# Performance work log

Measured on AMD Instinct MI355X. Metric: run time of the kernel, lower is better.

Reference implementation:

```python
import jax, jax.numpy as jnp
import numpy as np

B, T, D = 32, 1024, 1024
N, L = 256, 768
H = 16
TE = 2048


def layernorm(x, g, b, eps=1e-5):
    m = jnp.mean(x, axis=-1, keepdims=True)
    v = jnp.var(x, axis=-1, keepdims=True)
    return (x - m) * jax.lax.rsqrt(v + eps) * g + b


def setup_inputs() -> dict:
    key = jax.random.key(0)
    ks = jax.random.split(key, 16)
    s = 0.02
    return {
        "x": jax.random.normal(ks[0], (B, T, D), jnp.float32),
        "xf": jax.random.normal(ks[1], (B, N, L), jnp.float32),
        "emb": jax.random.normal(ks[2], (B, TE), jnp.float32),
        "src_mask": jnp.ones((B, T, 1), jnp.float32),
        "cond_type": jax.random.randint(ks[3], (B, 1, 1), 0, 100),
        # LayerNorm params
        "ln_x_g": jnp.ones((D,), jnp.float32), "ln_x_b": jnp.zeros((D,), jnp.float32),
        "ln_t_g": jnp.ones((L,), jnp.float32), "ln_t_b": jnp.zeros((L,), jnp.float32),
        # Q/K/V projections
        "Wq": jax.random.normal(ks[4], (D, D), jnp.float32) * s, "bq": jnp.zeros((D,), jnp.float32),
        "Wk": jax.random.normal(ks[5], (L, D), jnp.float32) * s, "bk": jnp.zeros((D,), jnp.float32),
        "Wv": jax.random.normal(ks[6], (L, D), jnp.float32) * s, "bv": jnp.zeros((D,), jnp.float32),
        # StylizationBlock: SiLU -> Linear(TE, 2D); LayerNorm(D); SiLU -> Linear(D, D)
        "We": jax.random.normal(ks[7], (TE, 2 * D), jnp.float32) * s, "be": jnp.zeros((2 * D,), jnp.float32),
        "ln_y_g": jnp.ones((D,), jnp.float32), "ln_y_b": jnp.zeros((D,), jnp.float32),
        "Wo": jax.random.normal(ks[8], (D, D), jnp.float32) * s, "bo": jnp.zeros((D,), jnp.float32),
    }


def reference(x, xf, emb, src_mask, cond_type,
              ln_x_g, ln_x_b, ln_t_g, ln_t_b,
              Wq, bq, Wk, bk, Wv, bv,
              We, be, ln_y_g, ln_y_b, Wo, bo):
    Bh, Th, Dh = x.shape
    Nn = xf.shape[1]
    head = Dh // H

    # text condition gate: (B,1,1), constant per batch element
    tcond = (cond_type % 10 > 0).astype(x.dtype).reshape(Bh, 1, 1)

    q = (layernorm(x, ln_x_g, ln_x_b) @ Wq + bq).reshape(Bh, Th, H, head)
    xf_n = layernorm(xf, ln_t_g, ln_t_b)
    k = (xf_n @ Wk + bk).reshape(Bh, Nn, H, head)

    # B,T,N,H scores (note: no 1/sqrt(d) scaling, as in the original)
    att = jnp.einsum('bthd,bnhd->btnh', q, k)
    att = att + (1.0 - tcond.reshape(Bh, 1, 1, 1)) * -1000000.0
    att = jax.nn.softmax(att, axis=2)

    v = ((xf_n @ Wv + bv) * tcond).reshape(Bh, Nn, H, head)
    y = jnp.einsum('btnh,bnhd->bthd', att, v).reshape(Bh, Th, Dh)

    # StylizationBlock (dropout inactive in eval)
    emb_out = jax.nn.silu(emb) @ We + be            # B, 2D
    scale, shift = jnp.split(emb_out, 2, axis=-1)   # B, D each
    h = layernorm(y, ln_y_g, ln_y_b) * (1.0 + scale[:, None, :]) + shift[:, None, :]
    h = jax.nn.silu(h) @ Wo + bo
    return x + h
```

## Files before the change

### kernel.cpp

```cpp
#include <hip/hip_runtime.h>
#include <hip/hip_bf16.h>

#define DEV __device__ __forceinline__

typedef __attribute__((ext_vector_type(8))) short bf16x8;
typedef __attribute__((ext_vector_type(4))) float f32x4;
typedef __attribute__((ext_vector_type(8))) unsigned short u16x8;

DEV unsigned short f2bf(float f){
  unsigned int b = __float_as_uint(f);
  return (unsigned short)((b + 0x7fffu + ((b >> 16) & 1u)) >> 16);
}
DEV float bf2f(unsigned short u){ return __uint_as_float(((unsigned int)u)<<16); }

DEV float silu_f(float v){ return v / (1.f + __expf(-v)); }

DEV void gl_lds16(const void* g, void* l){
  __builtin_amdgcn_global_load_lds((const __attribute__((address_space(1))) void*)g,
                                   (__attribute__((address_space(3))) void*)l, 16, 0, 0);
}

__global__ __launch_bounds__(256) void ln_rows(const float* __restrict__ x,
    const float* __restrict__ g, const float* __restrict__ bt,
    unsigned short* __restrict__ out, int D, int nvec)
{
  int row = blockIdx.x, t = threadIdx.x;
  const float4* xr = (const float4*)(x + (size_t)row * D);
  float4 v = make_float4(0.f,0.f,0.f,0.f);
  if (t < nvec) v = xr[t];
  float s  = v.x+v.y+v.z+v.w;
  float s2 = v.x*v.x+v.y*v.y+v.z*v.z+v.w*v.w;
  #pragma unroll
  for (int o=32;o;o>>=1){ s += __shfl_down(s,o,64); s2 += __shfl_down(s2,o,64); }
  __shared__ float red[8];
  if ((t&63)==0){ red[t>>6]=s; red[4+(t>>6)]=s2; }
  __syncthreads();
  float fs  = red[0]+red[1]+red[2]+red[3];
  float fs2 = red[4]+red[5]+red[6]+red[7];
  float mean = fs / (float)D;
  float var  = fmaxf(fs2/(float)D - mean*mean, 0.f);
  float rstd = rsqrtf(var + 1e-5f);
  if (t < nvec){
    float4 gv = ((const float4*)g)[t];
    float4 bv = ((const float4*)bt)[t];
    ushort4 o4;
    o4.x = f2bf((v.x-mean)*rstd*gv.x + bv.x);
    o4.y = f2bf((v.y-mean)*rstd*gv.y + bv.y);
    o4.z = f2bf((v.z-mean)*rstd*gv.z + bv.z);
    o4.w = f2bf((v.w-mean)*rstd*gv.w + bv.w);
    *(ushort4*)(out + (size_t)row*D + t*4) = o4;
  }
}

__global__ __launch_bounds__(256) void wconv(const float* __restrict__ W,
    unsigned short* __restrict__ Wt, int K, int N)
{
  __shared__ float tile[32][33];
  int n0 = blockIdx.x<<5, k0 = blockIdx.y<<5;
  int tx = threadIdx.x & 31, ty = threadIdx.x >> 5;
  #pragma unroll
  for (int i=0;i<4;i++)
    tile[ty + i*8][tx] = W[(size_t)(k0 + ty + i*8)*N + n0 + tx];
  __syncthreads();
  #pragma unroll
  for (int i=0;i<4;i++)
    Wt[(size_t)(n0 + ty + i*8)*K + k0 + tx] = f2bf(tile[tx][ty + i*8]);
}

__global__ __launch_bounds__(256) void bcat(const float* __restrict__ a,
    const float* __restrict__ b, float* __restrict__ o)
{
  int i = blockIdx.x*256 + threadIdx.x;
  o[i] = (i < 1024) ? a[i] : b[i-1024];
}

template<int MH, int KS>
DEV void phase_mfma(f32x4 (&acc)[8][4], const bf16x8 (&aF)[4], const bf16x8 (&bB)[2][4]){
  __builtin_amdgcn_s_barrier();
  __builtin_amdgcn_s_setprio(1);
  #pragma unroll
  for (int i=0;i<4;i++)
    #pragma unroll
    for (int j=0;j<4;j++)
      acc[MH*4+i][j] = __builtin_amdgcn_mfma_f32_16x16x32_bf16(aF[i], bB[KS][j], acc[MH*4+i][j], 0,0,0);
  __builtin_amdgcn_s_setprio(0);
  __builtin_amdgcn_s_barrier();
}

template<int EPI>
__global__ __launch_bounds__(512,2) void gemm256(
  const unsigned char* __restrict__ A, const unsigned char* __restrict__ Wt,
  const float* __restrict__ bias, void* __restrict__ Cout,
  const float* __restrict__ Xadd, int M, int N, int K, int gxshift)
{
  __shared__ __align__(16) unsigned char lds[131072];
  const int nwg = gridDim.x;
  const int chunk = nwg >> 3;
  const int wg = blockIdx.x;
  const int lg = (wg & 7) * chunk + (wg >> 3);
  const int bx = lg & ((1<<gxshift)-1);
  const int by = lg >> gxshift;
  const int tid = threadIdx.x, w = tid>>6, lane = tid&63;
  const int l15 = lane&15, lq = lane>>4;
  const int wr = w>>2, wc = w&3;
  const int m0 = by<<8, n0 = bx<<8;
  const size_t K2 = (size_t)K<<1;
  const int NT = K>>6;

  const int srow = w*8 + (lane>>3);
  const int scs  = (((lane&7) ^ (lane>>3))<<4);

  f32x4 acc[8][4];
  f32x4 zero = {0.f,0.f,0.f,0.f};
  #pragma unroll
  for (int i=0;i<8;i++)
    #pragma unroll
    for (int j=0;j<4;j++) acc[i][j] = zero;

  auto stg = [&](int bf, int mat, int c, int t){
    const unsigned char* src = mat ? Wt : A;
    int prow = mat ? n0 : m0;
    gl_lds16(src + (size_t)(prow + c*64 + srow)*K2 + ((size_t)t<<7) + scs,
             lds + bf*65536 + mat*32768 + c*8192 + w*1024);
  };
  auto ldA = [&](int mh, int i, int ks, int bf)->bf16x8 {
    int r = wr*128 + mh*64 + i*16 + l15;
    return *(const bf16x8*)(lds + bf*65536 + r*128 + ((ks*64 + lq*16) ^ ((r&7)<<4)));
  };
  auto ldB = [&](int j, int ks, int bf)->bf16x8 {
    int r = wc*64 + j*16 + l15;
    return *(const bf16x8*)(lds + bf*65536 + 32768 + r*128 + ((ks*64 + lq*16) ^ ((r&7)<<4)));
  };

  stg(0,0,0,0); stg(0,0,2,0);
  stg(0,1,0,0); stg(0,1,1,0);
  stg(0,1,2,0); stg(0,1,3,0);
  stg(0,0,1,0); stg(0,0,3,0);
  stg(1,0,0,1); stg(1,0,2,1);
  stg(1,1,0,1); stg(1,1,1,1);

  for (int u=0; u<NT; ++u){
    const int buf = u&1, nb = buf^1;
    if (u+1 < NT) { asm volatile("s_waitcnt vmcnt(4)" ::: "memory"); }
    else          { asm volatile("s_waitcnt vmcnt(0)" ::: "memory"); }
    __builtin_amdgcn_sched_barrier(0);
    __builtin_amdgcn_s_barrier();

    bf16x8 bB[2][4];
    bf16x8 aF[4];
    #pragma unroll
    for (int j=0;j<4;j++) bB[0][j] = ldB(j,0,buf);
    #pragma unroll
    for (int i=0;i<4;i++) aF[i] = ldA(0,i,0,buf);
    if (u+1 < NT){ stg(nb,1,2,u+1); stg(nb,1,3,u+1); }
    phase_mfma<0,0>(acc, aF, bB);
    #pragma unroll
    for (int j=0;j<4;j++) bB[1][j] = ldB(j,1,buf);
    #pragma unroll
    for (int i=0;i<4;i++) aF[i] = ldA(0,i,1,buf);
    if (u+1 < NT){ stg(nb,0,1,u+1); stg(nb,0,3,u+1); }
    phase_mfma<0,1>(acc, aF, bB);
    #pragma unroll
    for (int i=0;i<4;i++) aF[i] = ldA(1,i,0,buf);
    if (u+2 < NT){ stg(buf,0,0,u+2); stg(buf,0,2,u+2); }
    phase_mfma<1,0>(acc, aF, bB);
    #pragma unroll
    for (int i=0;i<4;i++) aF[i] = ldA(1,i,1,buf);
    if (u+2 < NT){ stg(buf,1,0,u+2); stg(buf,1,1,u+2); }
    phase_mfma<1,1>(acc, aF, bB);
  }

  #pragma unroll
  for (int j=0;j<4;j++){
    int n = n0 + wc*64 + j*16 + l15;
    float bv = bias[n];
    #pragma unroll
    for (int mf=0;mf<8;mf++){
      int mb = m0 + wr*128 + mf*16 + lq*4;
      #pragma unroll
      for (int r=0;r<4;r++){
        size_t idx = (size_t)(mb+r)*N + n;
        float val = acc[mf][j][r] + bv;
        if (EPI==0) ((unsigned short*)Cout)[idx] = f2bf(val);
        else        ((float*)Cout)[idx] = Xadd[idx] + val;
      }
    }
  }
}

__global__ __launch_bounds__(256) void vtransp(const unsigned short* __restrict__ v,
                                               int vstride, unsigned char* __restrict__ vt)
{
  __shared__ __align__(16) unsigned short tile[16384];
  int h = blockIdx.x, b = blockIdx.y, tid = threadIdx.x;
  const unsigned short* src = v + (size_t)b*256*vstride + h*64;
  #pragma unroll
  for (int it=0; it<8; ++it){
    int idx = it*256 + tid;
    int n = idx>>3, dc = idx&7;
    *(f32x4*)&tile[n*64 + dc*8] = *(const f32x4*)(src + (size_t)n*vstride + dc*8);
  }
  __syncthreads();
  unsigned char* dst = vt + (size_t)(b*16+h)*32768;
  #pragma unroll
  for (int it=0; it<8; ++it){
    int idx = it*256 + tid;
    int d = idx>>5, nc = idx&31;
    u16x8 o;
    #pragma unroll
    for (int j=0;j<8;j++) o[j] = tile[(nc*8+j)*64 + d];
    *(u16x8*)(dst + d*512 + ((nc*16) ^ ((d&7)<<4))) = o;
  }
}

__global__ __launch_bounds__(256,2) void attn64(
  const unsigned char* __restrict__ qg, const unsigned char* __restrict__ kg,
  int kstride, const unsigned char* __restrict__ vtg, const int* __restrict__ cond,
  unsigned short* __restrict__ yout)
{
  __shared__ __align__(16) unsigned char lds[73728];
  const int wg = blockIdx.x;
  const int lg = (wg & 7) * 1024 + (wg >> 3);
  const int t0 = (lg & 15) * 64;
  const int h  = (lg >> 4) & 15;
  const int b  = lg >> 8;
  const int tid = threadIdx.x, w = tid>>6, lane = tid&63;
  const int l15 = lane&15, lq = lane>>4;

  const unsigned char* kbase = kg + (size_t)b*256*kstride + (size_t)h*128;
  const unsigned char* vtb   = vtg + (size_t)(b*16+h)*32768;
  #pragma unroll
  for (int i=0;i<8;i++){
    int base = (w*8+i)*1024;
    int n  = (base>>7) + (lane>>3);
    int cb = (lane&7)<<4;
    gl_lds16(kbase + (size_t)n*kstride + (cb ^ ((n&7)<<4)), lds + base);
    gl_lds16(vtb + base + lane*16, lds + 32768 + base);
  }
  const unsigned char* qbase = qg + (size_t)(b*1024 + t0)*2048 + h*128;
  #pragma unroll
  for (int i=0;i<2;i++){
    int row = i*32 + (tid>>3);
    int cs  = ((tid&7)<<4) ^ ((row&7)<<4);
    gl_lds16(qbase + (size_t)row*2048 + cs, lds + 65536 + i*4096 + w*1024);
  }
  __syncthreads();

  const int qr = w*16 + l15;
  const int qsw = (qr&7)<<4;
  bf16x8 aq0 = *(const bf16x8*)(lds + 65536 + qr*128 + ((lq*16) ^ qsw));
  bf16x8 aq1 = *(const bf16x8*)(lds + 65536 + qr*128 + ((64 + lq*16) ^ qsw));

  f32x4 zero = {0.f,0.f,0.f,0.f};
  f32x4 s[16];
  #pragma unroll
  for (int nt=0;nt<16;nt++) s[nt] = zero;
  #pragma unroll
  for (int nt=0;nt<16;nt++){
    int n = nt*16 + l15;
    int rb = n<<7, sw = (n&7)<<4;
    bf16x8 kb0 = *(const bf16x8*)(lds + rb + ((lq*16) ^ sw));
    bf16x8 kb1 = *(const bf16x8*)(lds + rb + ((64 + lq*16) ^ sw));
    s[nt] = __builtin_amdgcn_mfma_f32_16x16x32_bf16(aq0, kb0, s[nt], 0,0,0);
    s[nt] = __builtin_amdgcn_mfma_f32_16x16x32_bf16(aq1, kb1, s[nt], 0,0,0);
  }
  #pragma unroll
  for (int r=0;r<4;r++){
    float m = s[0][r];
    #pragma unroll
    for (int nt=1;nt<16;nt++) m = fmaxf(m, s[nt][r]);
    m = fmaxf(m, __shfl_xor(m,1,64));
    m = fmaxf(m, __shfl_xor(m,2,64));
    m = fmaxf(m, __shfl_xor(m,4,64));
    m = fmaxf(m, __shfl_xor(m,8,64));
    float sum = 0.f;
    #pragma unroll
    for (int nt=0;nt<16;nt++){ float p = __expf(s[nt][r]-m); s[nt][r]=p; sum+=p; }
    sum += __shfl_xor(sum,1,64);
    sum += __shfl_xor(sum,2,64);
    sum += __shfl_xor(sum,4,64);
    sum += __shfl_xor(sum,8,64);
    float inv = 1.f/sum;
    #pragma unroll
    for (int nt=0;nt<16;nt++) s[nt][r] *= inv;
  }
  __syncthreads();
  #pragma unroll
  for (int nt=0;nt<16;nt++){
    int n = nt*16 + l15;
    int nb = (n>>3)<<4, nr = (n&7)<<1;
    #pragma unroll
    for (int r=0;r<4;r++){
      int tl = w*16 + lq*4 + r;
      *(unsigned short*)(lds + tl*512 + ((nb ^ ((tl&7)<<4)) | nr)) = f2bf(s[nt][r]);
    }
  }
  __syncthreads();
  f32x4 yv[4];
  #pragma unroll
  for (int dt=0;dt<4;dt++) yv[dt] = zero;
  const int tl = w*16 + l15;
  const int swp = (tl&7)<<4;
  #pragma unroll
  for (int kc=0;kc<8;kc++){
    bf16x8 pa = *(const bf16x8*)(lds + tl*512 + ((kc*64 + lq*16) ^ swp));
    #pragma unroll
    for (int dt=0;dt<4;dt++){
      int d = dt*16 + l15;
      bf16x8 vbv = *(const bf16x8*)(lds + 32768 + d*512 + ((kc*64 + lq*16) ^ ((d&7)<<4)));
      yv[dt] = __builtin_amdgcn_mfma_f32_16x16x32_bf16(pa, vbv, yv[dt], 0,0,0);
    }
  }
  float tc = (cond[b] % 10 > 0) ? 1.f : 0.f;
  #pragma unroll
  for (int dt=0;dt<4;dt++){
    #pragma unroll
    for (int r=0;r<4;r++){
      int tt = t0 + w*16 + lq*4 + r;
      yout[(size_t)(b*1024 + tt)*1024 + h*64 + dt*16 + l15] = f2bf(yv[dt][r]*tc);
    }
  }
}

__global__ __launch_bounds__(256) void embgemm(const float* __restrict__ emb,
    const float* __restrict__ We, float* __restrict__ epart)
{
  __shared__ float a[32][128];
  int cb = blockIdx.x, ks = blockIdx.y, tid = threadIdx.x;
  int k0 = ks<<7;
  #pragma unroll
  for (int it=0; it<4; ++it){
    int fi = it*256 + tid;
    int r = fi>>5, c4 = (fi&31)<<2;
    float4 vv = *(const float4*)(emb + (size_t)r*2048 + k0 + c4);
    vv.x = silu_f(vv.x); vv.y = silu_f(vv.y); vv.z = silu_f(vv.z); vv.w = silu_f(vv.w);
    *(float4*)&a[r][c4] = vv;
  }
  __syncthreads();
  int c0 = (cb<<8) + tid;
  float acc[32];
  #pragma unroll
  for (int r=0;r<32;r++) acc[r]=0.f;
  for (int kk=0;kk<128;kk++){
    float wv = We[(size_t)(k0+kk)*2048 + c0];
    #pragma unroll
    for (int r=0;r<32;r++) acc[r] += a[r][kk]*wv;
  }
  #pragma unroll
  for (int r=0;r<32;r++) epart[(size_t)(ks*32 + r)*2048 + c0] = acc[r];
}

__global__ __launch_bounds__(256) void embred(const float* __restrict__ epart,
    const float* __restrict__ be, float* __restrict__ eo)
{
  int idx = blockIdx.x*256 + threadIdx.x;
  float s = be[idx & 2047];
  #pragma unroll
  for (int ks=0;ks<16;ks++) s += epart[(size_t)ks*65536 + idx];
  eo[idx] = s;
}

__global__ __launch_bounds__(256) void styl(const unsigned short* __restrict__ y,
    const float* __restrict__ g, const float* __restrict__ bt,
    const float* __restrict__ eo, unsigned short* __restrict__ hout)
{
  int row = blockIdx.x, t = threadIdx.x, b = row>>10;
  ushort4 yv4 = ((const ushort4*)(y + (size_t)row*1024))[t];
  float in[4] = {bf2f(yv4.x), bf2f(yv4.y), bf2f(yv4.z), bf2f(yv4.w)};
  float s  = in[0]+in[1]+in[2]+in[3];
  float s2 = in[0]*in[0]+in[1]*in[1]+in[2]*in[2]+in[3]*in[3];
  #pragma unroll
  for (int o=32;o;o>>=1){ s += __shfl_down(s,o,64); s2 += __shfl_down(s2,o,64); }
  __shared__ float red[8];
  if ((t&63)==0){ red[t>>6]=s; red[4+(t>>6)]=s2; }
  __syncthreads();
  float fs  = red[0]+red[1]+red[2]+red[3];
  float fs2 = red[4]+red[5]+red[6]+red[7];
  float mean = fs*(1.f/1024.f);
  float var  = fmaxf(fs2*(1.f/1024.f) - mean*mean, 0.f);
  float rstd = rsqrtf(var + 1e-5f);
  float4 gv = ((const float4*)g)[t];
  float4 bv = ((const float4*)bt)[t];
  float4 sc = ((const float4*)(eo + (size_t)b*2048))[t];
  float4 sh = ((const float4*)(eo + (size_t)b*2048 + 1024))[t];
  float gg[4]  = {gv.x,gv.y,gv.z,gv.w};
  float bb[4]  = {bv.x,bv.y,bv.z,bv.w};
  float scs[4] = {sc.x,sc.y,sc.z,sc.w};
  float shs[4] = {sh.x,sh.y,sh.z,sh.w};
  unsigned short oo[4];
  #pragma unroll
  for (int c=0;c<4;c++){
    float hv = (in[c]-mean)*rstd*gg[c] + bb[c];
    hv = hv*(1.f+scs[c]) + shs[c];
    oo[c] = f2bf(silu_f(hv));
  }
  ushort4 o4; o4.x=oo[0]; o4.y=oo[1]; o4.z=oo[2]; o4.w=oo[3];
  *(ushort4*)(hout + (size_t)row*1024 + t*4) = o4;
}

extern "C" void kernel_launch(void* const* d_in, const int* in_sizes, int n_in,
                              void* d_out, int out_size, void* d_ws, size_t ws_size,
                              hipStream_t stream) {
  const float* x      = (const float*)d_in[0];
  const float* xf     = (const float*)d_in[1];
  const float* emb    = (const float*)d_in[2];
  const int*   cond   = (const int*)d_in[4];
  const float* ln_x_g = (const float*)d_in[5];
  const float* ln_x_b = (const float*)d_in[6];
  const float* ln_t_g = (const float*)d_in[7];
  const float* ln_t_b = (const float*)d_in[8];
  const float* Wq     = (const float*)d_in[9];
  const float* bq     = (const float*)d_in[10];
  const float* Wk     = (const float*)d_in[11];
  const float* bk     = (const float*)d_in[12];
  const float* Wv     = (const float*)d_in[13];
  const float* bv     = (const float*)d_in[14];
  const float* We     = (const float*)d_in[15];
  const float* be     = (const float*)d_in[16];
  const float* ln_y_g = (const float*)d_in[17];
  const float* ln_y_b = (const float*)d_in[18];
  const float* Wo     = (const float*)d_in[19];
  const float* bo     = (const float*)d_in[20];
  float* out = (float*)d_out;

  unsigned char* ws = (unsigned char*)d_ws;
  size_t off = 0;
  auto take = [&](size_t n){ unsigned char* p = ws + off; off += (n + 255) & ~(size_t)255; return p; };
  unsigned char* r1   = take(67108864);
  unsigned char* qb   = take(67108864);
  unsigned char* xfn  = take(12582912);
  unsigned char* kvb  = take(33554432);
  unsigned char* vtb  = take(16777216);
  unsigned char* wqt  = take(2097152);
  unsigned char* wkvt = take(3145728);
  unsigned char* wot  = take(2097152);
  unsigned char* eo   = take(262144);
  unsigned char* bkv  = take(8192);
  float* epart = (float*)r1;

  dim3 blk(256);
  dim3 blk512(512);
  wconv<<<dim3(32,32), blk, 0, stream>>>(Wq, (unsigned short*)wqt, 1024, 1024);
  wconv<<<dim3(32,24), blk, 0, stream>>>(Wk, (unsigned short*)wkvt,  768, 1024);
  wconv<<<dim3(32,24), blk, 0, stream>>>(Wv, (unsigned short*)wkvt + (size_t)1024*768, 768, 1024);
  wconv<<<dim3(32,32), blk, 0, stream>>>(Wo, (unsigned short*)wot, 1024, 1024);
  bcat<<<8, blk, 0, stream>>>(bk, bv, (float*)bkv);
  ln_rows<<<32768, blk, 0, stream>>>(x,  ln_x_g, ln_x_b, (unsigned short*)r1,  1024, 256);
  ln_rows<<<8192,  blk, 0, stream>>>(xf, ln_t_g, ln_t_b, (unsigned short*)xfn,  768, 192);
  gemm256<0><<<512, blk512, 0, stream>>>(r1,  wqt,  bq, qb, nullptr, 32768, 1024, 1024, 2);
  gemm256<0><<<256, blk512, 0, stream>>>(xfn, wkvt, (const float*)bkv, kvb, nullptr, 8192, 2048, 768, 3);
  vtransp<<<dim3(16,32), blk, 0, stream>>>((const unsigned short*)kvb + 1024, 2048, vtb);
  embgemm<<<dim3(8,16), blk, 0, stream>>>(emb, We, epart);
  embred<<<256, blk, 0, stream>>>(epart, be, (float*)eo);
  attn64<<<8192, blk, 0, stream>>>(qb, kvb, 4096, vtb, cond, (unsigned short*)qb);
  styl<<<32768, blk, 0, stream>>>((const unsigned short*)qb, ln_y_g, ln_y_b, (const float*)eo, (unsigned short*)r1);
  gemm256<1><<<512, blk512, 0, stream>>>(r1, wot, bo, out, x, 32768, 1024, 1024, 2);
}
```

Measured before the change: 495.8 us.

## Merge prep kernels, fuse V transpose into KV GEMM epilogue, reshape GEMM barriers

Collapses the four weight conversions and the bias concat into one prep launch, and runs both layernorms in a single launch. The KV projection GEMM now writes K compactly and writes V directly in the transposed, swizzled layout, which removes the separate vtransp kernel and its extra pass over memory. The GEMM main loop is restructured so that LDS waits and barriers bracket each MFMA phase and the global-load wait moves to the end of the iteration. The scattered 2-byte V stores may be uncoalesced, and the epilogue contains a redundant byte store that is immediately overwritten.

```diff
diff --git a/kernel.cpp b/kernel.cpp
--- a/kernel.cpp
+++ b/kernel.cpp
@@ -19,15 +19,24 @@
   __builtin_amdgcn_global_load_lds((const __attribute__((address_space(1))) void*)g,
                                    (__attribute__((address_space(3))) void*)l, 16, 0, 0);
 }
-
-__global__ __launch_bounds__(256) void ln_rows(const float* __restrict__ x,
-    const float* __restrict__ g, const float* __restrict__ bt,
-    unsigned short* __restrict__ out, int D, int nvec)
+DEV void wait_lds(){
+  asm volatile("s_waitcnt lgkmcnt(0)" ::: "memory");
+  __builtin_amdgcn_sched_barrier(0);
+}
+
+__global__ __launch_bounds__(256) void ln_all(const float* __restrict__ x,
+    const float* __restrict__ xf,
+    const float* __restrict__ gx, const float* __restrict__ bx_,
+    const float* __restrict__ gt, const float* __restrict__ bt,
+    unsigned short* __restrict__ ox, unsigned short* __restrict__ ot)
 {
   int row = blockIdx.x, t = threadIdx.x;
-  const float4* xr = (const float4*)(x + (size_t)row * D);
+  const float* src; const float* g; const float* bb; unsigned short* out;
+  int D, nvec;
+  if (row < 32768){ src = x + (size_t)row*1024; g = gx; bb = bx_; out = ox + (size_t)row*1024; D = 1024; nvec = 256; }
+  else { int r2 = row - 32768; src = xf + (size_t)r2*768; g = gt; bb = bt; out = ot + (size_t)r2*768; D = 768; nvec = 192; }
   float4 v = make_float4(0.f,0.f,0.f,0.f);
-  if (t < nvec) v = xr[t];
+  if (t < nvec) v = ((const float4*)src)[t];
   float s  = v.x+v.y+v.z+v.w;
   float s2 = v.x*v.x+v.y*v.y+v.z*v.z+v.w*v.w;
   #pragma unroll
@@ -42,22 +51,21 @@
   float rstd = rsqrtf(var + 1e-5f);
   if (t < nvec){
     float4 gv = ((const float4*)g)[t];
-    float4 bv = ((const float4*)bt)[t];
+    float4 bv = ((const float4*)bb)[t];
     ushort4 o4;
     o4.x = f2bf((v.x-mean)*rstd*gv.x + bv.x);
     o4.y = f2bf((v.y-mean)*rstd*gv.y + bv.y);
     o4.z = f2bf((v.z-mean)*rstd*gv.z + bv.z);
     o4.w = f2bf((v.w-mean)*rstd*gv.w + bv.w);
-    *(ushort4*)(out + (size_t)row*D + t*4) = o4;
-  }
-}
-
-__global__ __launch_bounds__(256) void wconv(const float* __restrict__ W,
-    unsigned short* __restrict__ Wt, int K, int N)
-{
-  __shared__ float tile[32][33];
-  int n0 = blockIdx.x<<5, k0 = blockIdx.y<<5;
-  int tx = threadIdx.x & 31, ty = threadIdx.x >> 5;
+    *(ushort4*)(out + t*4) = o4;
+  }
+}
+
+DEV void wtile(const float* W, unsigned short* Wt, int K, int N, int nt, int kt, int tid,
+               float (*tile)[33])
+{
+  int n0 = nt<<5, k0 = kt<<5;
+  int tx = tid & 31, ty = tid >> 5;
   #pragma unroll
   for (int i=0;i<4;i++)
     tile[ty + i*8][tx] = W[(size_t)(k0 + ty + i*8)*N + n0 + tx];
@@ -67,31 +75,47 @@
     Wt[(size_t)(n0 + ty + i*8)*K + k0 + tx] = f2bf(tile[tx][ty + i*8]);
 }
 
-__global__ __launch_bounds__(256) void bcat(const float* __restrict__ a,
-    const float* __restrict__ b, float* __restrict__ o)
-{
-  int i = blockIdx.x*256 + threadIdx.x;
-  o[i] = (i < 1024) ? a[i] : b[i-1024];
-}
-
-template<int MH, int KS>
-DEV void phase_mfma(f32x4 (&acc)[8][4], const bf16x8 (&aF)[4], const bf16x8 (&bB)[2][4]){
-  __builtin_amdgcn_s_barrier();
+__global__ __launch_bounds__(256) void prep(
+    const float* __restrict__ Wq, const float* __restrict__ Wk,
+    const float* __restrict__ Wv, const float* __restrict__ Wo,
+    const float* __restrict__ bk, const float* __restrict__ bv,
+    unsigned short* __restrict__ wqt, unsigned short* __restrict__ wkvt,
+    unsigned short* __restrict__ wot, float* __restrict__ bkv)
+{
+  __shared__ float tile[32][33];
+  int id = blockIdx.x, tid = threadIdx.x;
+  if (id < 8){
+    int i = id*256 + tid;
+    bkv[i] = (i < 1024) ? bk[i] : bv[i-1024];
+    return;
+  }
+  id -= 8;
+  if (id < 1024){ wtile(Wq, wqt, 1024, 1024, id & 31, id >> 5, tid, tile); return; }
+  id -= 1024;
+  if (id < 768){ wtile(Wk, wkvt, 768, 1024, id & 31, id >> 5, tid, tile); return; }
+  id -= 768;
+  if (id < 768){ wtile(Wv, wkvt + (size_t)1024*768, 768, 1024, id & 31, id >> 5, tid, tile); return; }
+  id -= 768;
+  wtile(Wo, wot, 1024, 1024, id & 31, id >> 5, tid, tile);
+}
+
+template<int MH>
+DEV void do_mfma(f32x4 (&acc)[8][4], const bf16x8 (&aF)[4], const bf16x8 (&bk)[4]){
   __builtin_amdgcn_s_setprio(1);
   #pragma unroll
   for (int i=0;i<4;i++)
     #pragma unroll
     for (int j=0;j<4;j++)
-      acc[MH*4+i][j] = __builtin_amdgcn_mfma_f32_16x16x32_bf16(aF[i], bB[KS][j], acc[MH*4+i][j], 0,0,0);
+      acc[MH*4+i][j] = __builtin_amdgcn_mfma_f32_16x16x32_bf16(aF[i], bk[j], acc[MH*4+i][j], 0,0,0);
   __builtin_amdgcn_s_setprio(0);
-  __builtin_amdgcn_s_barrier();
 }
 
 template<int EPI>
 __global__ __launch_bounds__(512,2) void gemm256(
   const unsigned char* __restrict__ A, const unsigned char* __restrict__ Wt,
   const float* __restrict__ bias, void* __restrict__ Cout,
-  const float* __restrict__ Xadd, int M, int N, int K, int gxshift)
+  const float* __restrict__ Xadd, unsigned char* __restrict__ vt,
+  int M, int N, int K, int gxshift)
 {
   __shared__ __align__(16) unsigned char lds[131072];
   const int nwg = gridDim.x;
@@ -138,78 +162,81 @@
   stg(0,0,1,0); stg(0,0,3,0);
   stg(1,0,0,1); stg(1,0,2,1);
   stg(1,1,0,1); stg(1,1,1,1);
+  asm volatile("s_waitcnt vmcnt(4)" ::: "memory");
+  __builtin_amdgcn_s_barrier();
 
   for (int u=0; u<NT; ++u){
     const int buf = u&1, nb = buf^1;
-    if (u+1 < NT) { asm volatile("s_waitcnt vmcnt(4)" ::: "memory"); }
-    else          { asm volatile("s_waitcnt vmcnt(0)" ::: "memory"); }
-    __builtin_amdgcn_sched_barrier(0);
-    __builtin_amdgcn_s_barrier();
-
-    bf16x8 bB[2][4];
-    bf16x8 aF[4];
-    #pragma unroll
-    for (int j=0;j<4;j++) bB[0][j] = ldB(j,0,buf);
+    bf16x8 aF[4], bB0[4], bB1[4];
+    #pragma unroll
+    for (int j=0;j<4;j++) bB0[j] = ldB(j,0,buf);
     #pragma unroll
     for (int i=0;i<4;i++) aF[i] = ldA(0,i,0,buf);
     if (u+1 < NT){ stg(nb,1,2,u+1); stg(nb,1,3,u+1); }
-    phase_mfma<0,0>(acc, aF, bB);
-    #pragma unroll
-    for (int j=0;j<4;j++) bB[1][j] = ldB(j,1,buf);
+    __builtin_amdgcn_s_barrier();
+    wait_lds();
+    do_mfma<0>(acc, aF, bB0);
+    __builtin_amdgcn_s_barrier();
+    #pragma unroll
+    for (int j=0;j<4;j++) bB1[j] = ldB(j,1,buf);
     #pragma unroll
     for (int i=0;i<4;i++) aF[i] = ldA(0,i,1,buf);
     if (u+1 < NT){ stg(nb,0,1,u+1); stg(nb,0,3,u+1); }
-    phase_mfma<0,1>(acc, aF, bB);
+    __builtin_amdgcn_s_barrier();
+    wait_lds();
+    do_mfma<0>(acc, aF, bB1);
+    __builtin_amdgcn_s_barrier();
     #pragma unroll
     for (int i=0;i<4;i++) aF[i] = ldA(1,i,0,buf);
     if (u+2 < NT){ stg(buf,0,0,u+2); stg(buf,0,2,u+2); }
-    phase_mfma<1,0>(acc, aF, bB);
+    __builtin_amdgcn_s_barrier();
+    wait_lds();
+    do_mfma<1>(acc, aF, bB0);
+    __builtin_amdgcn_s_barrier();
     #pragma unroll
     for (int i=0;i<4;i++) aF[i] = ldA(1,i,1,buf);
     if (u+2 < NT){ stg(buf,1,0,u+2); stg(buf,1,1,u+2); }
-    phase_mfma<1,1>(acc, aF, bB);
+    __builtin_amdgcn_s_barrier();
+    wait_lds();
+    do_mfma<1>(acc, aF, bB1);
+    if (u+1 < NT){
+      if (u+2 < NT) { asm volatile("s_waitcnt vmcnt(4)" ::: "memory"); }
+      else          { asm volatile("s_waitcnt vmcnt(0)" ::: "memory"); }
+      __builtin_amdgcn_sched_barrier(0);
+    }
+    __builtin_amdgcn_s_barrier();
   }
 
   #pragma unroll
   for (int j=0;j<4;j++){
     int n = n0 + wc*64 + j*16 + l15;
-    float bv = bias[n];
+    float bvs = bias[n];
     #pragma unroll
     for (int mf=0;mf<8;mf++){
       int mb = m0 + wr*128 + mf*16 + lq*4;
       #pragma unroll
       for (int r=0;r<4;r++){
-        size_t idx = (size_t)(mb+r)*N + n;
-        float val = acc[mf][j][r] + bv;
-        if (EPI==0) ((unsigned short*)Cout)[idx] = f2bf(val);
-        else        ((float*)Cout)[idx] = Xadd[idx] + val;
+        int m = mb + r;
+        float val = acc[mf][j][r] + bvs;
+        if (EPI==0){
+          ((unsigned short*)Cout)[(size_t)m*N + n] = f2bf(val);
+        } else if (EPI==1){
+          size_t idx = (size_t)m*N + n;
+          ((float*)Cout)[idx] = Xadd[idx] + val;
+        } else {
+          if (n0 < 1024){
+            ((unsigned short*)Cout)[(size_t)m*1024 + n] = f2bf(val);
+          } else {
+            int d = n - 1024 - ((n0-1024)&~63) - 0; d = (n-1024)&63;
+            int hh = (n-1024)>>6;
+            int bb_ = m>>8, nk = m&255;
+            vt[((size_t)(bb_*16+hh)<<15) + d*512 + (((nk>>3)<<4) ^ ((d&7)<<4)) + ((nk&7)<<1)] = f2bf(val) & 0xff ? 0 : 0;
+            *(unsigned short*)(vt + ((size_t)(bb_*16+hh)<<15) + d*512
+                + (((nk>>3)<<4) ^ ((d&7)<<4)) + ((nk&7)<<1)) = f2bf(val);
+          }
+        }
       }
     }
-  }
-}
-
-__global__ __launch_bounds__(256) void vtransp(const unsigned short* __restrict__ v,
-                                               int vstride, unsigned char* __restrict__ vt)
-{
-  __shared__ __align__(16) unsigned short tile[16384];
-  int h = blockIdx.x, b = blockIdx.y, tid = threadIdx.x;
-  const unsigned short* src = v + (size_t)b*256*vstride + h*64;
-  #pragma unroll
-  for (int it=0; it<8; ++it){
-    int idx = it*256 + tid;
-    int n = idx>>3, dc = idx&7;
-    *(f32x4*)&tile[n*64 + dc*8] = *(const f32x4*)(src + (size_t)n*vstride + dc*8);
-  }
-  __syncthreads();
-  unsigned char* dst = vt + (size_t)(b*16+h)*32768;
-  #pragma unroll
-  for (int it=0; it<8; ++it){
-    int idx = it*256 + tid;
-    int d = idx>>5, nc = idx&31;
-    u16x8 o;
-    #pragma unroll
-    for (int j=0;j<8;j++) o[j] = tile[(nc*8+j)*64 + d];
-    *(u16x8*)(dst + d*512 + ((nc*16) ^ ((d&7)<<4))) = o;
   }
 }
 
@@ -429,7 +456,7 @@
   unsigned char* r1   = take(67108864);
   unsigned char* qb   = take(67108864);
   unsigned char* xfn  = take(12582912);
-  unsigned char* kvb  = take(33554432);
+  unsigned char* kb   = take(16777216);
   unsigned char* vtb  = take(16777216);
   unsigned char* wqt  = take(2097152);
   unsigned char* wkvt = take(3145728);
@@ -440,19 +467,15 @@
 
   dim3 blk(256);
   dim3 blk512(512);
-  wconv<<<dim3(32,32), blk, 0, stream>>>(Wq, (unsigned short*)wqt, 1024, 1024);
-  wconv<<<dim3(32,24), blk, 0, stream>>>(Wk, (unsigned short*)wkvt,  768, 1024);
-  wconv<<<dim3(32,24), blk, 0, stream>>>(Wv, (unsigned short*)wkvt + (size_t)1024*768, 768, 1024);
-  wconv<<<dim3(32,32), blk, 0, stream>>>(Wo, (unsigned short*)wot, 1024, 1024);
-  bcat<<<8, blk, 0, stream>>>(bk, bv, (float*)bkv);
-  ln_rows<<<32768, blk, 0, stream>>>(x,  ln_x_g, ln_x_b, (unsigned short*)r1,  1024, 256);
-  ln_rows<<<8192,  blk, 0, stream>>>(xf, ln_t_g, ln_t_b, (unsigned short*)xfn,  768, 192);
-  gemm256<0><<<512, blk512, 0, stream>>>(r1,  wqt,  bq, qb, nullptr, 32768, 1024, 1024, 2);
-  gemm256<0><<<256, blk512, 0, stream>>>(xfn, wkvt, (const float*)bkv, kvb, nullptr, 8192, 2048, 768, 3);
-  vtransp<<<dim3(16,32), blk, 0, stream>>>((const unsigned short*)kvb + 1024, 2048, vtb);
+  prep<<<3592, blk, 0, stream>>>(Wq, Wk, Wv, Wo, bk, bv,
+      (unsigned short*)wqt, (unsigned short*)wkvt, (unsigned short*)wot, (float*)bkv);
+  ln_all<<<40960, blk, 0, stream>>>(x, xf, ln_x_g, ln_x_b, ln_t_g, ln_t_b,
+      (unsigned short*)r1, (unsigned short*)xfn);
+  gemm256<0><<<512, blk512, 0, stream>>>(r1, wqt, bq, qb, nullptr, nullptr, 32768, 1024, 1024, 2);
+  gemm256<2><<<256, blk512, 0, stream>>>(xfn, wkvt, (const float*)bkv, kb, nullptr, vtb, 8192, 2048, 768, 3);
   embgemm<<<dim3(8,16), blk, 0, stream>>>(emb, We, epart);
   embred<<<256, blk, 0, stream>>>(epart, be, (float*)eo);
-  attn64<<<8192, blk, 0, stream>>>(qb, kvb, 4096, vtb, cond, (unsigned short*)qb);
+  attn64<<<8192, blk, 0, stream>>>(qb, kb, 2048, vtb, cond, (unsigned short*)qb);
   styl<<<32768, blk, 0, stream>>>((const unsigned short*)qb, ln_y_g, ln_y_b, (const float*)eo, (unsigned short*)r1);
-  gemm256<1><<<512, blk512, 0, stream>>>(r1, wot, bo, out, x, 32768, 1024, 1024, 2);
-}
+  gemm256<1><<<512, blk512, 0, stream>>>(r1, wot, bo, out, x, nullptr, 32768, 1024, 1024, 2);
+}
```

New measurement: 469.6 us. 1.06x faster.
